# Kernel optimization log

Hardware: AMD Instinct MI355X
Metric: run time of the kernel (lower is better)

## Reference

```python
import jax, jax.numpy as jnp
import numpy as np

B, T = 1024, 128
LEN_VOCAB, IPD_VOCAB = 1500, 256
LEN_EB, IPD_EB = 64, 64
RNN_IN, HIDDEN, LABELS = 128, 512, 100


def setup_inputs() -> dict:
    key = jax.random.key(0)
    ks = jax.random.split(key, 11)
    std = 1.0 / np.sqrt(HIDDEN)

    def u(k, shape, s):
        return jax.random.uniform(k, shape, jnp.float32, -s, s)

    return {
        "x": jax.random.randint(ks[0], (B, T, 2), 0, 256, dtype=jnp.int64),
        "len_emb": jax.random.normal(ks[1], (LEN_VOCAB, LEN_EB), jnp.float32),
        "ipd_emb": jax.random.normal(ks[2], (IPD_VOCAB, IPD_EB), jnp.float32),
        "fc1_w": u(ks[3], (RNN_IN, LEN_EB + IPD_EB), 1.0 / np.sqrt(LEN_EB + IPD_EB)),
        "fc1_b": u(ks[4], (RNN_IN,), 1.0 / np.sqrt(LEN_EB + IPD_EB)),
        "x2h_w": u(ks[5], (HIDDEN, RNN_IN), std),
        "x2h_b": u(ks[6], (HIDDEN,), std),
        "h2h_w": u(ks[7], (HIDDEN, HIDDEN), std),
        "h2h_b": u(ks[8], (HIDDEN,), std),
        "fc2_w": u(ks[9], (LABELS, HIDDEN), 1.0 / np.sqrt(HIDDEN)),
        "fc2_b": u(ks[10], (LABELS,), 1.0 / np.sqrt(HIDDEN)),
    }


def reference(x, len_emb, ipd_emb, fc1_w, fc1_b, x2h_w, x2h_b, h2h_w, h2h_b, fc2_w, fc2_b):
    # Embedding lookups: [B, T, 64] each -> concat [B, T, 128]
    feats = jnp.concatenate([len_emb[x[:, :, 0]], ipd_emb[x[:, :, 1]]], axis=-1)
    # fc1 then precompute the x2h part of the recurrence for all timesteps
    r = feats @ fc1_w.T + fc1_b                       # [B, T, RNN_IN]
    xin = r @ x2h_w.T + x2h_b                         # [B, T, HIDDEN]
    xin_t = jnp.swapaxes(xin, 0, 1)                   # [T, B, HIDDEN]

    def step(h, xt):
        h = jnp.tanh(xt + h @ h2h_w.T + h2h_b)
        return h, None

    h0 = jnp.zeros((x.shape[0], h2h_w.shape[0]), dtype=xin.dtype)
    h_last, _ = jax.lax.scan(step, h0, xin_t)
    # eval mode: dropout is identity
    return h_last @ fc2_w.T + fc2_b                   # [B, LABELS]
```

## Files before the change

kernel.cpp:

```cpp
#include <hip/hip_runtime.h>

#define B_SZ 1024
#define T_SZ 128
#define HID 512
#define LAB 100

#define OFF_XC    0u
#define OFF_WH    262144u
#define OFF_FC2   786432u
#define OFF_FC2B  888832u
#define OFF_WEFFT 889344u
#define OFF_BEFF  1151488u
#define OFF_ELEN  1153536u
#define OFF_EIPD  1415680u
#define WS_NEED   1677824u

typedef __attribute__((ext_vector_type(8))) short short8;
typedef __attribute__((ext_vector_type(4))) float float4v;
typedef __attribute__((ext_vector_type(4))) unsigned short us4;
typedef __attribute__((ext_vector_type(8))) __bf16 bf8_t;
typedef unsigned long long ull;

__device__ __attribute__((aligned(16))) unsigned char g_blob[WS_NEED];

__device__ __forceinline__ float bf2f(unsigned short u) {
    union { unsigned int i; float f; } z; z.i = ((unsigned int)u) << 16; return z.f;
}
__device__ __forceinline__ unsigned short f2bf(float f) {
    union { float f; unsigned int i; } z; z.f = f;
    unsigned int r = z.i + 0x7FFFu + ((z.i >> 16) & 1u);
    return (unsigned short)(r >> 16);
}
__device__ __forceinline__ float4v mfma16(short8 a, short8 b, float4v c) {
    return __builtin_amdgcn_mfma_f32_16x16x32_bf16(
        __builtin_bit_cast(bf8_t, a), __builtin_bit_cast(bf8_t, b), c, 0, 0, 0);
}

__launch_bounds__(256)
__global__ void k1_kernel(const float* __restrict__ fc1_f, const float* __restrict__ fc1b_f,
                          const float* __restrict__ x2h_f, const float* __restrict__ x2hb_f,
                          const float* __restrict__ h2hb_f,
                          float* __restrict__ wefft, float* __restrict__ beff) {
    const int tid = threadIdx.x;
    if (blockIdx.x < 64) {
        int gid = blockIdx.x * 256 + tid;
        int n  = gid >> 5;
        int k0 = (gid & 31) * 4;
        const float* xr = x2h_f + n * 128;
        float a0 = 0.f, a1 = 0.f, a2 = 0.f, a3 = 0.f;
#pragma unroll 4
        for (int j = 0; j < 128; j++) {
            float xv = xr[j];
            float4v fv = *(const float4v*)(fc1_f + j * 128 + k0);
            a0 += xv * fv[0]; a1 += xv * fv[1];
            a2 += xv * fv[2]; a3 += xv * fv[3];
        }
        wefft[(k0 + 0) * 512 + n] = a0;
        wefft[(k0 + 1) * 512 + n] = a1;
        wefft[(k0 + 2) * 512 + n] = a2;
        wefft[(k0 + 3) * 512 + n] = a3;
        return;
    }
    int tg = (blockIdx.x - 64) * 256 + tid;
    float s = x2hb_f[tg] + h2hb_f[tg];
    const float4v* xr = (const float4v*)(x2h_f + tg * 128);
    const float4v* bb = (const float4v*)fc1b_f;
    for (int j = 0; j < 32; j++) {
        float4v a = xr[j], b = bb[j];
        s += a[0] * b[0] + a[1] * b[1] + a[2] * b[2] + a[3] * b[3];
    }
    beff[tg] = s;
}

__launch_bounds__(256)
__global__ void k2_kernel(const float* __restrict__ wefft, const float* __restrict__ beff,
                          const float* __restrict__ len_f, const float* __restrict__ ipd_f,
                          const int* __restrict__ xi, unsigned char* __restrict__ xc,
                          const float* __restrict__ h2h_f, const float* __restrict__ fc2_f,
                          const float* __restrict__ fc2b_f,
                          unsigned short* __restrict__ elen, unsigned short* __restrict__ eipd,
                          unsigned short* __restrict__ o_wh, unsigned short* __restrict__ o_fc2,
                          float* __restrict__ o_fc2b) {
    const int tid = threadIdx.x;
    if (blockIdx.x < 256) {
        int grp = blockIdx.x * 256 + tid;
        int tab = grp >> 15;
        int g2  = grp & 32767;
        int v   = g2 >> 7;
        int n0  = (g2 & 127) * 4;
        const float* emb = (tab ? ipd_f : len_f) + v * 64;
        const float* wt  = wefft + tab * 64 * 512 + n0;
        float a0 = 0.f, a1 = 0.f, a2 = 0.f, a3 = 0.f;
#pragma unroll 8
        for (int k = 0; k < 64; k++) {
            float e = emb[k];
            float4v w = *(const float4v*)(wt + k * 512);
            a0 += e * w[0]; a1 += e * w[1]; a2 += e * w[2]; a3 += e * w[3];
        }
        if (tab) {
            float4v b4 = *(const float4v*)&beff[n0];
            a0 += b4[0]; a1 += b4[1]; a2 += b4[2]; a3 += b4[3];
        }
        us4 o = { f2bf(a0), f2bf(a1), f2bf(a2), f2bf(a3) };
        unsigned short* dst = tab ? eipd : elen;
        *(us4*)&dst[v * 512 + n0] = o;
        return;
    }
    if (blockIdx.x < 512) {
        __shared__ int is64;
        if (tid == 0) {
            int nz = 0;
            for (int j = 1; j < 64; j += 2) nz |= xi[j];
            is64 = (nz == 0) ? 1 : 0;
        }
        __syncthreads();
        const int n = B_SZ * T_SZ * 2;
        const int i64 = is64;
        for (int i = (blockIdx.x - 256) * 256 + tid; i < n; i += 256 * 256) {
            int v = i64 ? xi[2 * i] : xi[i];
            v = v < 0 ? 0 : (v > 255 ? 255 : v);
            int b = i >> 8, r = i & 255, t = r >> 1, c = r & 1;
            xc[t * 2048 + b * 2 + c] = (unsigned char)v;
        }
        return;
    }
    const int N2 = 262144, N3 = 51200, N5 = 100;
    const int total = N2 + N3 + N5;
    for (int i = (blockIdx.x - 512) * 256 + tid; i < total; i += 613 * 256) {
        int j = i;
        if (j < N2) { o_wh[j] = f2bf(h2h_f[j]); continue; }
        j -= N2;
        if (j < N3) { o_fc2[j] = f2bf(fc2_f[j]); continue; }
        j -= N3;
        o_fc2b[j] = fc2b_f[j];
    }
}

__launch_bounds__(512, 2)
__global__ void rnn_kernel(const unsigned short* __restrict__ w_wh,
                           const unsigned char* __restrict__ w_xc,
                           const unsigned short* __restrict__ w_elen,
                           const unsigned short* __restrict__ w_eipd,
                           const unsigned short* __restrict__ w_fc2,
                           const float* __restrict__ w_fc2b,
                           float* __restrict__ out) {
    extern __shared__ unsigned short sm2[];
    unsigned short* sA = sm2;
    unsigned short* sH = sm2 + 65536;

    const int tid  = threadIdx.x;
    const int wv   = tid >> 6;
    const int ln   = tid & 63;
    const int mcol = ln & 15;
    const int q    = ln >> 4;
    const int g    = blockIdx.x;
    const int b0   = g * 16;
    const int n0   = wv * 64;

    for (int it = 0; it < 16; it++) {
        int chunk = it * 512 + tid;
        int r = chunk >> 4, c = chunk & 15;
        uint4 v = *(const uint4*)(w_wh + r * 512 + 384 + c * 8);
        *(uint4*)&sA[r * 128 + ((c ^ (r & 15)) & 15) * 8] = v;
    }
    {
        uint4 z = {0, 0, 0, 0};
        *(uint4*)&sH[tid * 8] = z;
        *(uint4*)&sH[(512 + tid) * 8] = z;
    }
    short8 whr[4][12];
#pragma unroll
    for (int nt = 0; nt < 4; nt++)
#pragma unroll
        for (int kt = 0; kt < 12; kt++)
            whr[nt][kt] = *(const short8*)(w_wh + (n0 + nt * 16 + mcol) * 512 + kt * 32 + q * 8);

    const int qlo = (q ^ (mcol & 3)) * 8;
    int ej[4];
#pragma unroll
    for (int j = 0; j < 4; j++)
        ej[j] = ((j * 4) ^ (mcol & 12)) * 8;
    const int base_b = mcol * 512 + qlo;
    const int fbase  = (n0 + mcol) * 128 + qlo;
    int hw_off[4];
#pragma unroll
    for (int nt = 0; nt < 4; nt++) {
        int n = n0 + nt * 16 + q * 4;
        hw_off[nt] = mcol * 512 + (((n >> 3) ^ mcol) & 63) * 8 + (n & 7);
    }

    const int xb2  = (b0 + mcol) * 2;
    const int ecol = n0 + q * 4;
    us4 tq[4], ti[4];
    {
        unsigned int i0 = *(const unsigned short*)&w_xc[xb2];
        const unsigned short* eL = w_elen + (i0 & 255u) * 512 + ecol;
        const unsigned short* eI = w_eipd + (i0 >> 8) * 512 + ecol;
#pragma unroll
        for (int nt = 0; nt < 4; nt++) {
            tq[nt] = *(const us4*)(eL + nt * 16);
            ti[nt] = *(const us4*)(eI + nt * 16);
        }
    }
    unsigned int idxP = *(const unsigned short*)&w_xc[2048 + xb2];

    __syncthreads();

    for (int t = 0; t < T_SZ; t++) {
        const unsigned short* hRd = sH + ((t & 1) << 13);
        unsigned short* hWr = sH + (((t + 1) & 1) << 13);

        float4v acc[4];
#pragma unroll
        for (int nt = 0; nt < 4; nt++) {
            acc[nt][0] = bf2f(tq[nt][0]) + bf2f(ti[nt][0]);
            acc[nt][1] = bf2f(tq[nt][1]) + bf2f(ti[nt][1]);
            acc[nt][2] = bf2f(tq[nt][2]) + bf2f(ti[nt][2]);
            acc[nt][3] = bf2f(tq[nt][3]) + bf2f(ti[nt][3]);
        }
        if (t + 1 < T_SZ) {
            const unsigned short* eL = w_elen + (idxP & 255u) * 512 + ecol;
            const unsigned short* eI = w_eipd + (idxP >> 8) * 512 + ecol;
#pragma unroll
            for (int nt = 0; nt < 4; nt++) {
                tq[nt] = *(const us4*)(eL + nt * 16);
                ti[nt] = *(const us4*)(eI + nt * 16);
            }
            if (t + 2 < T_SZ)
                idxP = *(const unsigned short*)&w_xc[(t + 2) * 2048 + xb2];
        }

#pragma unroll
        for (int kt = 0; kt < 12; kt++) {
            short8 bh = *(const short8*)&hRd[base_b + ej[kt & 3] + (kt >> 2) * 128];
#pragma unroll
            for (int nt = 0; nt < 4; nt++)
                acc[nt] = mfma16(whr[nt][kt], bh, acc[nt]);
        }
#pragma unroll
        for (int j = 0; j < 4; j++) {
            short8 bh = *(const short8*)&hRd[base_b + ej[j] + 384];
#pragma unroll
            for (int nt = 0; nt < 4; nt++) {
                short8 fa = *(const short8*)&sA[fbase + nt * 2048 + ej[j]];
                acc[nt] = mfma16(fa, bh, acc[nt]);
            }
        }

#pragma unroll
        for (int nt = 0; nt < 4; nt++) {
            unsigned short o[4];
#pragma unroll
            for (int r = 0; r < 4; r++) {
                float e  = __expf(2.0f * acc[nt][r]);
                float th = 1.0f - 2.0f * __builtin_amdgcn_rcpf(e + 1.0f);
                o[r] = f2bf(th);
            }
            us4 v4 = { o[0], o[1], o[2], o[3] };
            *(us4*)&hWr[hw_off[nt]] = v4;
        }
        __syncthreads();
    }

    unsigned short* hF = sH;

    if (wv < 7) {
        int lA = wv * 16 + mcol; if (lA > 99) lA = 99;
        float4v a2 = {0.f, 0.f, 0.f, 0.f};
#pragma unroll
        for (int kt = 0; kt < 16; kt++) {
            short8 fa = *(const short8*)(w_fc2 + lA * 512 + kt * 32 + q * 8);
            short8 bh = *(const short8*)&hF[base_b + ej[kt & 3] + (kt >> 2) * 128];
            a2 = mfma16(fa, bh, a2);
        }
#pragma unroll
        for (int r = 0; r < 4; r++) {
            int l = wv * 16 + q * 4 + r;
            if (l < 100) out[(b0 + mcol) * 100 + l] = a2[r] + w_fc2b[l];
        }
    }
}

extern "C" void kernel_launch(void* const* d_in, const int* in_sizes, int n_in,
                              void* d_out, int out_size, void* d_ws, size_t ws_size,
                              hipStream_t stream) {
    unsigned char* base = (unsigned char*)d_ws;
    if (ws_size < (size_t)WS_NEED) {
        void* p = nullptr;
        hipGetSymbolAddress(&p, HIP_SYMBOL(g_blob));
        base = (unsigned char*)p;
    }
    unsigned char*  w_xc    = base + OFF_XC;
    unsigned short* w_wh    = (unsigned short*)(base + OFF_WH);
    unsigned short* w_fc2   = (unsigned short*)(base + OFF_FC2);
    float*          w_fc2b  = (float*)(base + OFF_FC2B);
    float*          w_wefft = (float*)(base + OFF_WEFFT);
    float*          w_beff  = (float*)(base + OFF_BEFF);
    unsigned short* w_elen  = (unsigned short*)(base + OFF_ELEN);
    unsigned short* w_eipd  = (unsigned short*)(base + OFF_EIPD);

    static bool attr_set = false;
    if (!attr_set) {
        hipFuncSetAttribute((const void*)rnn_kernel,
                            hipFuncAttributeMaxDynamicSharedMemorySize, 163840);
        attr_set = true;
    }

    k1_kernel<<<66, 256, 0, stream>>>(
        (const float*)d_in[3], (const float*)d_in[4],
        (const float*)d_in[5], (const float*)d_in[6], (const float*)d_in[8],
        w_wefft, w_beff);
    k2_kernel<<<1125, 256, 0, stream>>>(
        w_wefft, w_beff,
        (const float*)d_in[1], (const float*)d_in[2],
        (const int*)d_in[0], w_xc,
        (const float*)d_in[7], (const float*)d_in[9], (const float*)d_in[10],
        w_elen, w_eipd, w_wh, w_fc2, w_fc2b);
    rnn_kernel<<<64, 512, 163840, stream>>>(
        w_wh, w_xc, w_elen, w_eipd, w_fc2, w_fc2b, (float*)d_out);
}
```

Before: 397.1 us.

## Fuse precompute and RNN kernels into one persistent launch with flag-based sync

Merges the two preprocessing kernels and the RNN kernel into a single 192-block launch. Producer blocks signal completion through global atomic counters that consumer blocks spin on. The h2h and fc2 bf16 conversions move into the RNN blocks, which convert fp32 weights on load, and the embedding tables are written in a permuted layout so each lane fetches two 8-wide vectors instead of four 4-wide ones. This removes two kernel launches and the intermediate bf16 weight copies. In exchange it relies on all 192 blocks being co-resident (2 per CU with 160KB of LDS) to avoid deadlock, and adds a small zeroing kernel.

```diff
diff --git a/kernel.cpp b/kernel.cpp
--- a/kernel.cpp
+++ b/kernel.cpp
@@ -6,16 +6,15 @@
 #define LAB 100
 
 #define OFF_XC    0u
-#define OFF_WH    262144u
-#define OFF_FC2   786432u
-#define OFF_FC2B  888832u
-#define OFF_WEFFT 889344u
-#define OFF_BEFF  1151488u
-#define OFF_ELEN  1153536u
-#define OFF_EIPD  1415680u
-#define WS_NEED   1677824u
+#define OFF_WEFFT 262144u
+#define OFF_BEFF  524288u
+#define OFF_ELEN  526336u
+#define OFF_EIPD  788480u
+#define OFF_FLAGS 1050624u
+#define WS_NEED   1050640u
 
 typedef __attribute__((ext_vector_type(8))) short short8;
+typedef __attribute__((ext_vector_type(8))) unsigned short us8;
 typedef __attribute__((ext_vector_type(4))) float float4v;
 typedef __attribute__((ext_vector_type(4))) unsigned short us4;
 typedef __attribute__((ext_vector_type(8))) __bf16 bf8_t;
@@ -36,14 +35,28 @@
         __builtin_bit_cast(bf8_t, a), __builtin_bit_cast(bf8_t, b), c, 0, 0, 0);
 }
 
-__launch_bounds__(256)
-__global__ void k1_kernel(const float* __restrict__ fc1_f, const float* __restrict__ fc1b_f,
-                          const float* __restrict__ x2h_f, const float* __restrict__ x2hb_f,
-                          const float* __restrict__ h2hb_f,
-                          float* __restrict__ wefft, float* __restrict__ beff) {
+__global__ void zero_kernel(unsigned int* __restrict__ flags) {
+    if (threadIdx.x < 3) flags[threadIdx.x] = 0u;
+}
+
+__launch_bounds__(512, 2)
+__global__ void fused_kernel(const int* __restrict__ xi,
+                             const float* __restrict__ len_f, const float* __restrict__ ipd_f,
+                             const float* __restrict__ fc1_f, const float* __restrict__ fc1b_f,
+                             const float* __restrict__ x2h_f, const float* __restrict__ x2hb_f,
+                             const float* __restrict__ h2h_f, const float* __restrict__ h2hb_f,
+                             const float* __restrict__ fc2_f, const float* __restrict__ fc2b_f,
+                             unsigned char* __restrict__ xc,
+                             float* __restrict__ wefft, float* __restrict__ beff,
+                             unsigned short* __restrict__ elen, unsigned short* __restrict__ eipd,
+                             unsigned int* __restrict__ flags,
+                             float* __restrict__ out) {
+    extern __shared__ unsigned short sm2[];
     const int tid = threadIdx.x;
-    if (blockIdx.x < 64) {
-        int gid = blockIdx.x * 256 + tid;
+    const int b   = blockIdx.x;
+
+    if (b < 32) {
+        int gid = b * 512 + tid;
         int n  = gid >> 5;
         int k0 = (gid & 31) * 4;
         const float* xr = x2h_f + n * 128;
@@ -59,109 +72,111 @@
         wefft[(k0 + 1) * 512 + n] = a1;
         wefft[(k0 + 2) * 512 + n] = a2;
         wefft[(k0 + 3) * 512 + n] = a3;
+        __syncthreads();
+        if (tid == 0) {
+            __threadfence();
+            __hip_atomic_fetch_add(&flags[0], 1u, __ATOMIC_RELEASE, __HIP_MEMORY_SCOPE_SYSTEM);
+        }
         return;
     }
-    int tg = (blockIdx.x - 64) * 256 + tid;
-    float s = x2hb_f[tg] + h2hb_f[tg];
-    const float4v* xr = (const float4v*)(x2h_f + tg * 128);
-    const float4v* bb = (const float4v*)fc1b_f;
-    for (int j = 0; j < 32; j++) {
-        float4v a = xr[j], b = bb[j];
-        s += a[0] * b[0] + a[1] * b[1] + a[2] * b[2] + a[3] * b[3];
-    }
-    beff[tg] = s;
-}
-
-__launch_bounds__(256)
-__global__ void k2_kernel(const float* __restrict__ wefft, const float* __restrict__ beff,
-                          const float* __restrict__ len_f, const float* __restrict__ ipd_f,
-                          const int* __restrict__ xi, unsigned char* __restrict__ xc,
-                          const float* __restrict__ h2h_f, const float* __restrict__ fc2_f,
-                          const float* __restrict__ fc2b_f,
-                          unsigned short* __restrict__ elen, unsigned short* __restrict__ eipd,
-                          unsigned short* __restrict__ o_wh, unsigned short* __restrict__ o_fc2,
-                          float* __restrict__ o_fc2b) {
-    const int tid = threadIdx.x;
-    if (blockIdx.x < 256) {
-        int grp = blockIdx.x * 256 + tid;
-        int tab = grp >> 15;
-        int g2  = grp & 32767;
-        int v   = g2 >> 7;
-        int n0  = (g2 & 127) * 4;
-        const float* emb = (tab ? ipd_f : len_f) + v * 64;
-        const float* wt  = wefft + tab * 64 * 512 + n0;
-        float a0 = 0.f, a1 = 0.f, a2 = 0.f, a3 = 0.f;
-#pragma unroll 8
-        for (int k = 0; k < 64; k++) {
-            float e = emb[k];
-            float4v w = *(const float4v*)(wt + k * 512);
-            a0 += e * w[0]; a1 += e * w[1]; a2 += e * w[2]; a3 += e * w[3];
-        }
-        if (tab) {
-            float4v b4 = *(const float4v*)&beff[n0];
-            a0 += b4[0]; a1 += b4[1]; a2 += b4[2]; a3 += b4[3];
-        }
-        us4 o = { f2bf(a0), f2bf(a1), f2bf(a2), f2bf(a3) };
-        unsigned short* dst = tab ? eipd : elen;
-        *(us4*)&dst[v * 512 + n0] = o;
+    if (b == 32) {
+        float s = x2hb_f[tid] + h2hb_f[tid];
+        const float4v* xr = (const float4v*)(x2h_f + tid * 128);
+        const float4v* bb = (const float4v*)fc1b_f;
+        for (int j = 0; j < 32; j++) {
+            float4v a = xr[j], c = bb[j];
+            s += a[0] * c[0] + a[1] * c[1] + a[2] * c[2] + a[3] * c[3];
+        }
+        beff[tid] = s;
+        __syncthreads();
+        if (tid == 0) {
+            __threadfence();
+            __hip_atomic_fetch_add(&flags[0], 1u, __ATOMIC_RELEASE, __HIP_MEMORY_SCOPE_SYSTEM);
+        }
         return;
     }
-    if (blockIdx.x < 512) {
-        __shared__ int is64;
-        if (tid == 0) {
-            int nz = 0;
-            for (int j = 1; j < 64; j += 2) nz |= xi[j];
-            is64 = (nz == 0) ? 1 : 0;
-        }
-        __syncthreads();
+    if (b < 64) {
+        int nz = 0;
+        for (int j = 1; j < 64; j += 2) nz |= xi[j];
+        const int i64 = (nz == 0) ? 1 : 0;
         const int n = B_SZ * T_SZ * 2;
-        const int i64 = is64;
-        for (int i = (blockIdx.x - 256) * 256 + tid; i < n; i += 256 * 256) {
+        for (int i = (b - 33) * 512 + tid; i < n; i += 31 * 512) {
             int v = i64 ? xi[2 * i] : xi[i];
             v = v < 0 ? 0 : (v > 255 ? 255 : v);
-            int b = i >> 8, r = i & 255, t = r >> 1, c = r & 1;
-            xc[t * 2048 + b * 2 + c] = (unsigned char)v;
+            int bb2 = i >> 8, r = i & 255, t = r >> 1, c = r & 1;
+            xc[t * 2048 + bb2 * 2 + c] = (unsigned char)v;
+        }
+        __syncthreads();
+        if (tid == 0) {
+            __threadfence();
+            __hip_atomic_fetch_add(&flags[1], 1u, __ATOMIC_RELEASE, __HIP_MEMORY_SCOPE_SYSTEM);
         }
         return;
     }
-    const int N2 = 262144, N3 = 51200, N5 = 100;
-    const int total = N2 + N3 + N5;
-    for (int i = (blockIdx.x - 512) * 256 + tid; i < total; i += 613 * 256) {
-        int j = i;
-        if (j < N2) { o_wh[j] = f2bf(h2h_f[j]); continue; }
-        j -= N2;
-        if (j < N3) { o_fc2[j] = f2bf(fc2_f[j]); continue; }
-        j -= N3;
-        o_fc2b[j] = fc2b_f[j];
-    }
-}
-
-__launch_bounds__(512, 2)
-__global__ void rnn_kernel(const unsigned short* __restrict__ w_wh,
-                           const unsigned char* __restrict__ w_xc,
-                           const unsigned short* __restrict__ w_elen,
-                           const unsigned short* __restrict__ w_eipd,
-                           const unsigned short* __restrict__ w_fc2,
-                           const float* __restrict__ w_fc2b,
-                           float* __restrict__ out) {
-    extern __shared__ unsigned short sm2[];
+    if (b < 128) {
+        if (tid == 0) {
+            while (__hip_atomic_load(&flags[0], __ATOMIC_RELAXED, __HIP_MEMORY_SCOPE_SYSTEM) < 33u)
+                __builtin_amdgcn_s_sleep(8);
+            __threadfence();
+        }
+        __syncthreads();
+        int gid = (b - 64) * 512 + tid;
+#pragma unroll
+        for (int ii = 0; ii < 2; ii++) {
+            int grp = gid + ii * 32768;
+            int tab = grp >> 15;
+            int g2  = grp & 32767;
+            int v   = g2 >> 7;
+            int nq  = (g2 & 127) * 4;
+            const float* emb = (tab ? ipd_f : len_f) + v * 64;
+            const float* wt  = wefft + tab * 64 * 512 + nq;
+            float a0 = 0.f, a1 = 0.f, a2 = 0.f, a3 = 0.f;
+#pragma unroll 8
+            for (int k = 0; k < 64; k++) {
+                float e = emb[k];
+                float4v w = *(const float4v*)(wt + k * 512);
+                a0 += e * w[0]; a1 += e * w[1]; a2 += e * w[2]; a3 += e * w[3];
+            }
+            if (tab) {
+                float4v b4 = *(const float4v*)&beff[nq];
+                a0 += b4[0]; a1 += b4[1]; a2 += b4[2]; a3 += b4[3];
+            }
+            int nt = (nq >> 4) & 3, qq = (nq >> 2) & 3;
+            int p0 = (nq & ~63) + ((nt >> 1) << 5) + qq * 8 + ((nt & 1) << 2);
+            us4 o = { f2bf(a0), f2bf(a1), f2bf(a2), f2bf(a3) };
+            unsigned short* dst = tab ? eipd : elen;
+            *(us4*)&dst[v * 512 + p0] = o;
+        }
+        __syncthreads();
+        if (tid == 0) {
+            __threadfence();
+            __hip_atomic_fetch_add(&flags[2], 1u, __ATOMIC_RELEASE, __HIP_MEMORY_SCOPE_SYSTEM);
+        }
+        return;
+    }
+
     unsigned short* sA = sm2;
     unsigned short* sH = sm2 + 65536;
 
-    const int tid  = threadIdx.x;
     const int wv   = tid >> 6;
     const int ln   = tid & 63;
     const int mcol = ln & 15;
     const int q    = ln >> 4;
-    const int g    = blockIdx.x;
+    const int g    = b - 128;
     const int b0   = g * 16;
     const int n0   = wv * 64;
 
     for (int it = 0; it < 16; it++) {
         int chunk = it * 512 + tid;
         int r = chunk >> 4, c = chunk & 15;
-        uint4 v = *(const uint4*)(w_wh + r * 512 + 384 + c * 8);
-        *(uint4*)&sA[r * 128 + ((c ^ (r & 15)) & 15) * 8] = v;
+        const float* s = h2h_f + r * 512 + 384 + c * 8;
+        float4v a = *(const float4v*)s;
+        float4v d = *(const float4v*)(s + 4);
+        us4 lo = { f2bf(a[0]), f2bf(a[1]), f2bf(a[2]), f2bf(a[3]) };
+        us4 hi = { f2bf(d[0]), f2bf(d[1]), f2bf(d[2]), f2bf(d[3]) };
+        unsigned short* dst = &sA[r * 128 + ((c ^ (r & 15)) & 15) * 8];
+        *(us4*)dst = lo;
+        *(us4*)(dst + 4) = hi;
     }
     {
         uint4 z = {0, 0, 0, 0};
@@ -172,8 +187,14 @@
 #pragma unroll
     for (int nt = 0; nt < 4; nt++)
 #pragma unroll
-        for (int kt = 0; kt < 12; kt++)
-            whr[nt][kt] = *(const short8*)(w_wh + (n0 + nt * 16 + mcol) * 512 + kt * 32 + q * 8);
+        for (int kt = 0; kt < 12; kt++) {
+            const float* s = h2h_f + (n0 + nt * 16 + mcol) * 512 + kt * 32 + q * 8;
+            float4v a = *(const float4v*)s;
+            float4v d = *(const float4v*)(s + 4);
+            short8 w8 = { (short)f2bf(a[0]), (short)f2bf(a[1]), (short)f2bf(a[2]), (short)f2bf(a[3]),
+                          (short)f2bf(d[0]), (short)f2bf(d[1]), (short)f2bf(d[2]), (short)f2bf(d[3]) };
+            whr[nt][kt] = w8;
+        }
 
     const int qlo = (q ^ (mcol & 3)) * 8;
     int ej[4];
@@ -189,22 +210,25 @@
         hw_off[nt] = mcol * 512 + (((n >> 3) ^ mcol) & 63) * 8 + (n & 7);
     }
 
+    if (tid == 0) {
+        while (__hip_atomic_load(&flags[1], __ATOMIC_RELAXED, __HIP_MEMORY_SCOPE_SYSTEM) < 31u ||
+               __hip_atomic_load(&flags[2], __ATOMIC_RELAXED, __HIP_MEMORY_SCOPE_SYSTEM) < 64u)
+            __builtin_amdgcn_s_sleep(8);
+        __threadfence();
+    }
+    __syncthreads();
+
     const int xb2  = (b0 + mcol) * 2;
-    const int ecol = n0 + q * 4;
-    us4 tq[4], ti[4];
+    const int ecol = n0 + q * 8;
+    us8 tL0, tL1, tI0, tI1;
     {
-        unsigned int i0 = *(const unsigned short*)&w_xc[xb2];
-        const unsigned short* eL = w_elen + (i0 & 255u) * 512 + ecol;
-        const unsigned short* eI = w_eipd + (i0 >> 8) * 512 + ecol;
-#pragma unroll
-        for (int nt = 0; nt < 4; nt++) {
-            tq[nt] = *(const us4*)(eL + nt * 16);
-            ti[nt] = *(const us4*)(eI + nt * 16);
-        }
-    }
-    unsigned int idxP = *(const unsigned short*)&w_xc[2048 + xb2];
-
-    __syncthreads();
+        unsigned int i0 = *(const unsigned short*)&xc[xb2];
+        const unsigned short* eL = elen + (i0 & 255u) * 512 + ecol;
+        const unsigned short* eI = eipd + (i0 >> 8) * 512 + ecol;
+        tL0 = *(const us8*)eL;  tL1 = *(const us8*)(eL + 32);
+        tI0 = *(const us8*)eI;  tI1 = *(const us8*)(eI + 32);
+    }
+    unsigned int idxP = *(const unsigned short*)&xc[2048 + xb2];
 
     for (int t = 0; t < T_SZ; t++) {
         const unsigned short* hRd = sH + ((t & 1) << 13);
@@ -212,22 +236,19 @@
 
         float4v acc[4];
 #pragma unroll
-        for (int nt = 0; nt < 4; nt++) {
-            acc[nt][0] = bf2f(tq[nt][0]) + bf2f(ti[nt][0]);
-            acc[nt][1] = bf2f(tq[nt][1]) + bf2f(ti[nt][1]);
-            acc[nt][2] = bf2f(tq[nt][2]) + bf2f(ti[nt][2]);
-            acc[nt][3] = bf2f(tq[nt][3]) + bf2f(ti[nt][3]);
+        for (int r = 0; r < 4; r++) {
+            acc[0][r] = bf2f(tL0[r])     + bf2f(tI0[r]);
+            acc[1][r] = bf2f(tL0[4 + r]) + bf2f(tI0[4 + r]);
+            acc[2][r] = bf2f(tL1[r])     + bf2f(tI1[r]);
+            acc[3][r] = bf2f(tL1[4 + r]) + bf2f(tI1[4 + r]);
         }
         if (t + 1 < T_SZ) {
-            const unsigned short* eL = w_elen + (idxP & 255u) * 512 + ecol;
-            const unsigned short* eI = w_eipd + (idxP >> 8) * 512 + ecol;
-#pragma unroll
-            for (int nt = 0; nt < 4; nt++) {
-                tq[nt] = *(const us4*)(eL + nt * 16);
-                ti[nt] = *(const us4*)(eI + nt * 16);
-            }
+            const unsigned short* eL = elen + (idxP & 255u) * 512 + ecol;
+            const unsigned short* eI = eipd + (idxP >> 8) * 512 + ecol;
+            tL0 = *(const us8*)eL;  tL1 = *(const us8*)(eL + 32);
+            tI0 = *(const us8*)eI;  tI1 = *(const us8*)(eI + 32);
             if (t + 2 < T_SZ)
-                idxP = *(const unsigned short*)&w_xc[(t + 2) * 2048 + xb2];
+                idxP = *(const unsigned short*)&xc[(t + 2) * 2048 + xb2];
         }
 
 #pragma unroll
@@ -269,14 +290,18 @@
         float4v a2 = {0.f, 0.f, 0.f, 0.f};
 #pragma unroll
         for (int kt = 0; kt < 16; kt++) {
-            short8 fa = *(const short8*)(w_fc2 + lA * 512 + kt * 32 + q * 8);
+            const float* s = fc2_f + lA * 512 + kt * 32 + q * 8;
+            float4v fa0 = *(const float4v*)s;
+            float4v fa1 = *(const float4v*)(s + 4);
+            short8 fa = { (short)f2bf(fa0[0]), (short)f2bf(fa0[1]), (short)f2bf(fa0[2]), (short)f2bf(fa0[3]),
+                          (short)f2bf(fa1[0]), (short)f2bf(fa1[1]), (short)f2bf(fa1[2]), (short)f2bf(fa1[3]) };
             short8 bh = *(const short8*)&hF[base_b + ej[kt & 3] + (kt >> 2) * 128];
             a2 = mfma16(fa, bh, a2);
         }
 #pragma unroll
         for (int r = 0; r < 4; r++) {
             int l = wv * 16 + q * 4 + r;
-            if (l < 100) out[(b0 + mcol) * 100 + l] = a2[r] + w_fc2b[l];
+            if (l < 100) out[(b0 + mcol) * 100 + l] = a2[r] + fc2b_f[l];
         }
     }
 }
@@ -291,31 +316,27 @@
         base = (unsigned char*)p;
     }
     unsigned char*  w_xc    = base + OFF_XC;
-    unsigned short* w_wh    = (unsigned short*)(base + OFF_WH);
-    unsigned short* w_fc2   = (unsigned short*)(base + OFF_FC2);
-    float*          w_fc2b  = (float*)(base + OFF_FC2B);
     float*          w_wefft = (float*)(base + OFF_WEFFT);
     float*          w_beff  = (float*)(base + OFF_BEFF);
     unsigned short* w_elen  = (unsigned short*)(base + OFF_ELEN);
     unsigned short* w_eipd  = (unsigned short*)(base + OFF_EIPD);
+    unsigned int*   w_flags = (unsigned int*)(base + OFF_FLAGS);
 
     static bool attr_set = false;
     if (!attr_set) {
-        hipFuncSetAttribute((const void*)rnn_kernel,
+        hipFuncSetAttribute((const void*)fused_kernel,
                             hipFuncAttributeMaxDynamicSharedMemorySize, 163840);
         attr_set = true;
     }
 
-    k1_kernel<<<66, 256, 0, stream>>>(
+    zero_kernel<<<1, 64, 0, stream>>>(w_flags);
+    fused_kernel<<<192, 512, 163840, stream>>>(
+        (const int*)d_in[0],
+        (const float*)d_in[1], (const float*)d_in[2],
         (const float*)d_in[3], (const float*)d_in[4],
-        (const float*)d_in[5], (const float*)d_in[6], (const float*)d_in[8],
-        w_wefft, w_beff);
-    k2_kernel<<<1125, 256, 0, stream>>>(
-        w_wefft, w_beff,
-        (const float*)d_in[1], (const float*)d_in[2],
-        (const int*)d_in[0], w_xc,
-        (const float*)d_in[7], (const float*)d_in[9], (const float*)d_in[10],
-        w_elen, w_eipd, w_wh, w_fc2, w_fc2b);
-    rnn_kernel<<<64, 512, 163840, stream>>>(
-        w_wh, w_xc, w_elen, w_eipd, w_fc2, w_fc2b, (float*)d_out);
-}
+        (const float*)d_in[5], (const float*)d_in[6],
+        (const float*)d_in[7], (const float*)d_in[8],
+        (const float*)d_in[9], (const float*)d_in[10],
+        w_xc, w_wefft, w_beff, w_elen, w_eipd, w_flags,
+        (float*)d_out);
+}
```

New measurement: 462.7 us. 16.5% more time.
